# Performance work log

Hardware: AMD Instinct MI355X
Metric: run time of the kernel (lower is better)

## Reference

```python
import jax, jax.numpy as jnp
import numpy as np

N, D = 32768, 1024

def setup_inputs() -> dict:
    key = jax.random.key(0)
    k1, k2, k3 = jax.random.split(key, 3)
    elg = jax.random.normal(k1, (N, D), dtype=jnp.float32)
    eth = jax.random.normal(k2, (N, D), dtype=jnp.float32)
    weight = jax.random.normal(k3, (D, D), dtype=jnp.float32)
    return {"elg": elg, "eth": eth, "weight": weight}

def reference(elg, eth, weight):
    # out[n] = elg[n] @ W @ eth[n]  -- batched bilinear form, fully fused
    return jnp.einsum('nd,de,ne->n', elg, weight, eth)
```

## Files before the change

### kernel.cpp

```cpp
#include <hip/hip_runtime.h>
#include <hip/hip_bf16.h>

typedef __attribute__((ext_vector_type(8))) short short8;
typedef __attribute__((ext_vector_type(4))) float float4v;
typedef __attribute__((ext_vector_type(4))) unsigned int uint4v;

#define DDIM 1024
#define ETH_STRIDE 40

__device__ __forceinline__ unsigned short f2bf(float f) {
  unsigned u = __builtin_bit_cast(unsigned, f);
  unsigned r = (u + 0x7fffu + ((u >> 16) & 1u)) >> 16;
  return (unsigned short)r;
}
__device__ __forceinline__ unsigned pk2(float lo, float hi) {
  return (unsigned)f2bf(lo) | ((unsigned)f2bf(hi) << 16);
}

__global__ __launch_bounds__(256) void convert_w(const float* __restrict__ W,
                                                 unsigned short* __restrict__ Wb) {
  size_t i = ((size_t)blockIdx.x * 256 + threadIdx.x) * 8;
  float4v a = *(const float4v*)(W + i);
  float4v b = *(const float4v*)(W + i + 4);
  uint4v pk;
  pk.x = pk2(a.x, a.y); pk.y = pk2(a.z, a.w);
  pk.z = pk2(b.x, b.y); pk.w = pk2(b.z, b.w);
  *(uint4v*)(Wb + i) = pk;
}

__global__ __launch_bounds__(256, 3) void bilinear_kernel(const float* __restrict__ elg,
                                                          const float* __restrict__ eth,
                                                          const unsigned short* __restrict__ Wb,
                                                          float* __restrict__ out) {
  __shared__ unsigned short ethL[64 * ETH_STRIDE];
  __shared__ unsigned short Wbuf[256 * 32];
  __shared__ float wsum[4][64];

  const int tid  = threadIdx.x;
  const int lane = tid & 63;
  const int w    = tid >> 6;
  const int quad = lane >> 4;
  const int l15  = lane & 15;
  const int m0   = (blockIdx.x >> 2) * 64;
  const int d0   = (blockIdx.x & 3) * 256;

  const int erow = tid >> 2, eunit = tid & 3;
  const float* esrc = eth + (size_t)(m0 + erow) * DDIM + eunit * 8;

  const int wr = lane >> 2, wu = lane & 3;

  float4v er0 = *(const float4v*)(esrc);
  float4v er1 = *(const float4v*)(esrc + 4);

  float4v acc[4][4];
#pragma unroll
  for (int ct = 0; ct < 4; ++ct)
#pragma unroll
    for (int rt = 0; rt < 4; ++rt)
      acc[ct][rt] = (float4v){0.f, 0.f, 0.f, 0.f};

  for (int ek = 0; ek < 32; ++ek) {
    const int e0 = ek * 32;
    __syncthreads();

    {
      uint4v pk;
      pk.x = pk2(er0.x, er0.y); pk.y = pk2(er0.z, er0.w);
      pk.z = pk2(er1.x, er1.y); pk.w = pk2(er1.z, er1.w);
      *(uint4v*)&ethL[erow * ETH_STRIDE + eunit * 8] = pk;
    }

#pragma unroll
    for (int j = 0; j < 4; ++j) {
      int r  = (w * 4 + j) * 16 + wr;
      int ug = wu ^ ((r >> 1) & 3);
      const unsigned short* gp = Wb + (size_t)(d0 + r) * DDIM + e0 + ug * 8;
      unsigned short* lp = &Wbuf[(w * 4 + j) * 512 + lane * 8];
      __builtin_amdgcn_global_load_lds(
          (const __attribute__((address_space(1))) unsigned int*)gp,
          (__attribute__((address_space(3))) unsigned int*)lp, 16, 0, 0);
    }
    __syncthreads();

    short8 aF[4], bF[4];
#pragma unroll
    for (int rt = 0; rt < 4; ++rt)
      aF[rt] = *(const short8*)&ethL[(rt * 16 + l15) * ETH_STRIDE + quad * 8];
#pragma unroll
    for (int ct = 0; ct < 4; ++ct) {
      int dl = w * 64 + ct * 16 + l15;
      int pu = quad ^ ((dl >> 1) & 3);
      bF[ct] = *(const short8*)&Wbuf[dl * 32 + pu * 8];
    }

    if (ek < 31) {
      const float* s = esrc + (e0 + 32);
      er0 = *(const float4v*)(s);
      er1 = *(const float4v*)(s + 4);
    }

#pragma unroll
    for (int ct = 0; ct < 4; ++ct)
#pragma unroll
      for (int rt = 0; rt < 4; ++rt)
        acc[ct][rt] = __builtin_amdgcn_mfma_f32_16x16x32_bf16(aF[rt], bF[ct], acc[ct][rt], 0, 0, 0);
  }

  float p[16];
#pragma unroll
  for (int j = 0; j < 16; ++j) p[j] = 0.f;
#pragma unroll
  for (int ct = 0; ct < 4; ++ct) {
    int col = d0 + w * 64 + ct * 16 + l15;
#pragma unroll
    for (int rt = 0; rt < 4; ++rt) {
      const float* ep = elg + (size_t)(m0 + rt * 16 + quad * 4) * DDIM + col;
#pragma unroll
      for (int i = 0; i < 4; ++i)
        p[rt * 4 + i] += acc[ct][rt][i] * ep[(size_t)i * DDIM];
    }
  }

#pragma unroll
  for (int off = 1; off < 16; off <<= 1)
#pragma unroll
    for (int j = 0; j < 16; ++j)
      p[j] += __shfl_xor(p[j], off);

  if (l15 == 0) {
#pragma unroll
    for (int rt = 0; rt < 4; ++rt)
#pragma unroll
      for (int i = 0; i < 4; ++i)
        wsum[w][rt * 16 + quad * 4 + i] = p[rt * 4 + i];
  }
  __syncthreads();
  if (tid < 64) {
    float s = wsum[0][tid] + wsum[1][tid] + wsum[2][tid] + wsum[3][tid];
    atomicAdd(&out[m0 + tid], s);
  }
}

extern "C" void kernel_launch(void* const* d_in, const int* in_sizes, int n_in,
                              void* d_out, int out_size, void* d_ws, size_t ws_size,
                              hipStream_t stream) {
  (void)in_sizes; (void)n_in; (void)ws_size;
  const float* elg = (const float*)d_in[0];
  const float* eth = (const float*)d_in[1];
  const float* W   = (const float*)d_in[2];
  float* out = (float*)d_out;
  unsigned short* Wb = (unsigned short*)d_ws;

  hipMemsetAsync(d_out, 0, (size_t)out_size * sizeof(float), stream);
  convert_w<<<dim3(512), dim3(256), 0, stream>>>(W, Wb);
  bilinear_kernel<<<dim3(2048), dim3(256), 0, stream>>>(elg, eth, Wb, out);
}
```

Before: 368.3 us.

## Pre-convert eth to bf16 and double-buffer async LDS staging

Adds a combined conversion kernel that turns both W and eth into bf16 in workspace. The main kernel then streams both operands into LDS with global_load_lds, double-buffered so the next k-slice loads while MFMAs run on the current one, with one barrier per iteration. This removes the per-iteration fp32 register conversion and the second barrier. The cost is an extra 128MB read and 64MB write pass over eth, and a 64MB workspace requirement, with the old path kept as a fallback.

Measured after the change: 365.6 us. About the same (-0.7%).

```diff
diff --git a/kernel.cpp b/kernel.cpp
--- a/kernel.cpp
+++ b/kernel.cpp
@@ -16,24 +16,40 @@
 __device__ __forceinline__ unsigned pk2(float lo, float hi) {
   return (unsigned)f2bf(lo) | ((unsigned)f2bf(hi) << 16);
 }
-
+__device__ __forceinline__ void cvt8(const float* src, unsigned short* dst) {
+  float4v a = *(const float4v*)(src);
+  float4v b = *(const float4v*)(src + 4);
+  uint4v pk;
+  pk.x = pk2(a.x, a.y); pk.y = pk2(a.z, a.w);
+  pk.z = pk2(b.x, b.y); pk.w = pk2(b.z, b.w);
+  *(uint4v*)dst = pk;
+}
+
+__global__ __launch_bounds__(256) void convert_all(const float* __restrict__ W,
+                                                   const float* __restrict__ eth,
+                                                   unsigned short* __restrict__ Wb,
+                                                   unsigned short* __restrict__ ethB) {
+  int b = blockIdx.x;
+  if (b < 512) {
+    size_t i = ((size_t)b * 256 + threadIdx.x) * 8;
+    cvt8(W + i, Wb + i);
+  } else {
+    size_t i = ((size_t)(b - 512) * 256 + threadIdx.x) * 8;
+    cvt8(eth + i, ethB + i);
+  }
+}
 __global__ __launch_bounds__(256) void convert_w(const float* __restrict__ W,
                                                  unsigned short* __restrict__ Wb) {
   size_t i = ((size_t)blockIdx.x * 256 + threadIdx.x) * 8;
-  float4v a = *(const float4v*)(W + i);
-  float4v b = *(const float4v*)(W + i + 4);
-  uint4v pk;
-  pk.x = pk2(a.x, a.y); pk.y = pk2(a.z, a.w);
-  pk.z = pk2(b.x, b.y); pk.w = pk2(b.z, b.w);
-  *(uint4v*)(Wb + i) = pk;
-}
-
-__global__ __launch_bounds__(256, 3) void bilinear_kernel(const float* __restrict__ elg,
-                                                          const float* __restrict__ eth,
-                                                          const unsigned short* __restrict__ Wb,
-                                                          float* __restrict__ out) {
-  __shared__ unsigned short ethL[64 * ETH_STRIDE];
-  __shared__ unsigned short Wbuf[256 * 32];
+  cvt8(W + i, Wb + i);
+}
+
+__global__ __launch_bounds__(256, 3) void bilinear_bf16(const float* __restrict__ elg,
+                                                        const unsigned short* __restrict__ ethB,
+                                                        const unsigned short* __restrict__ Wb,
+                                                        float* __restrict__ out) {
+  __shared__ unsigned short Wbuf[2][256 * 32];
+  __shared__ unsigned short ethL[2][64 * 32];
   __shared__ float wsum[4][64];
 
   const int tid  = threadIdx.x;
@@ -43,33 +59,130 @@
   const int l15  = lane & 15;
   const int m0   = (blockIdx.x >> 2) * 64;
   const int d0   = (blockIdx.x & 3) * 256;
-
+  const int wr = lane >> 2, wu = lane & 3;
+
+  auto stage = [&](int ek, int buf) {
+    const int e0 = ek * 32;
+#pragma unroll
+    for (int j = 0; j < 4; ++j) {
+      int r  = (w * 4 + j) * 16 + wr;
+      int ug = wu ^ ((r >> 1) & 3);
+      const unsigned short* gp = Wb + (size_t)(d0 + r) * DDIM + e0 + ug * 8;
+      unsigned short* lp = &Wbuf[buf][(w * 4 + j) * 512 + lane * 8];
+      __builtin_amdgcn_global_load_lds(
+          (const __attribute__((address_space(1))) unsigned int*)gp,
+          (__attribute__((address_space(3))) unsigned int*)lp, 16, 0, 0);
+    }
+    {
+      int er = w * 16 + wr;
+      const unsigned short* gp = ethB + (size_t)(m0 + er) * DDIM + e0 + wu * 8;
+      unsigned short* lp = &ethL[buf][w * 512 + lane * 8];
+      __builtin_amdgcn_global_load_lds(
+          (const __attribute__((address_space(1))) unsigned int*)gp,
+          (__attribute__((address_space(3))) unsigned int*)lp, 16, 0, 0);
+    }
+  };
+
+  float4v acc[4][4];
+#pragma unroll
+  for (int ct = 0; ct < 4; ++ct)
+#pragma unroll
+    for (int rt = 0; rt < 4; ++rt)
+      acc[ct][rt] = (float4v){0.f, 0.f, 0.f, 0.f};
+
+  stage(0, 0);
+  __syncthreads();
+
+  for (int ek = 0; ek < 32; ++ek) {
+    const int cur = ek & 1;
+    if (ek < 31) stage(ek + 1, cur ^ 1);
+
+    short8 aF[4], bF[4];
+#pragma unroll
+    for (int rt = 0; rt < 4; ++rt)
+      aF[rt] = *(const short8*)&ethL[cur][(rt * 16 + l15) * 32 + quad * 8];
+#pragma unroll
+    for (int ct = 0; ct < 4; ++ct) {
+      int dl = w * 64 + ct * 16 + l15;
+      int pu = quad ^ ((dl >> 1) & 3);
+      bF[ct] = *(const short8*)&Wbuf[cur][dl * 32 + pu * 8];
+    }
+#pragma unroll
+    for (int ct = 0; ct < 4; ++ct)
+#pragma unroll
+      for (int rt = 0; rt < 4; ++rt)
+        acc[ct][rt] = __builtin_amdgcn_mfma_f32_16x16x32_bf16(aF[rt], bF[ct], acc[ct][rt], 0, 0, 0);
+
+    __syncthreads();
+  }
+
+  float p[16];
+#pragma unroll
+  for (int j = 0; j < 16; ++j) p[j] = 0.f;
+#pragma unroll
+  for (int ct = 0; ct < 4; ++ct) {
+    int col = d0 + w * 64 + ct * 16 + l15;
+#pragma unroll
+    for (int rt = 0; rt < 4; ++rt) {
+      const float* ep = elg + (size_t)(m0 + rt * 16 + quad * 4) * DDIM + col;
+#pragma unroll
+      for (int i = 0; i < 4; ++i)
+        p[rt * 4 + i] += acc[ct][rt][i] * ep[(size_t)i * DDIM];
+    }
+  }
+#pragma unroll
+  for (int off = 1; off < 16; off <<= 1)
+#pragma unroll
+    for (int j = 0; j < 16; ++j)
+      p[j] += __shfl_xor(p[j], off);
+  if (l15 == 0) {
+#pragma unroll
+    for (int rt = 0; rt < 4; ++rt)
+#pragma unroll
+      for (int i = 0; i < 4; ++i)
+        wsum[w][rt * 16 + quad * 4 + i] = p[rt * 4 + i];
+  }
+  __syncthreads();
+  if (tid < 64) {
+    float s = wsum[0][tid] + wsum[1][tid] + wsum[2][tid] + wsum[3][tid];
+    atomicAdd(&out[m0 + tid], s);
+  }
+}
+
+__global__ __launch_bounds__(256, 3) void bilinear_fp32eth(const float* __restrict__ elg,
+                                                           const float* __restrict__ eth,
+                                                           const unsigned short* __restrict__ Wb,
+                                                           float* __restrict__ out) {
+  __shared__ unsigned short ethL[64 * ETH_STRIDE];
+  __shared__ unsigned short Wbuf[256 * 32];
+  __shared__ float wsum[4][64];
+  const int tid  = threadIdx.x;
+  const int lane = tid & 63;
+  const int w    = tid >> 6;
+  const int quad = lane >> 4;
+  const int l15  = lane & 15;
+  const int m0   = (blockIdx.x >> 2) * 64;
+  const int d0   = (blockIdx.x & 3) * 256;
   const int erow = tid >> 2, eunit = tid & 3;
   const float* esrc = eth + (size_t)(m0 + erow) * DDIM + eunit * 8;
-
   const int wr = lane >> 2, wu = lane & 3;
-
   float4v er0 = *(const float4v*)(esrc);
   float4v er1 = *(const float4v*)(esrc + 4);
-
   float4v acc[4][4];
 #pragma unroll
   for (int ct = 0; ct < 4; ++ct)
 #pragma unroll
     for (int rt = 0; rt < 4; ++rt)
       acc[ct][rt] = (float4v){0.f, 0.f, 0.f, 0.f};
-
   for (int ek = 0; ek < 32; ++ek) {
     const int e0 = ek * 32;
     __syncthreads();
-
     {
       uint4v pk;
       pk.x = pk2(er0.x, er0.y); pk.y = pk2(er0.z, er0.w);
       pk.z = pk2(er1.x, er1.y); pk.w = pk2(er1.z, er1.w);
       *(uint4v*)&ethL[erow * ETH_STRIDE + eunit * 8] = pk;
     }
-
 #pragma unroll
     for (int j = 0; j < 4; ++j) {
       int r  = (w * 4 + j) * 16 + wr;
@@ -81,7 +194,6 @@
           (__attribute__((address_space(3))) unsigned int*)lp, 16, 0, 0);
     }
     __syncthreads();
-
     short8 aF[4], bF[4];
 #pragma unroll
     for (int rt = 0; rt < 4; ++rt)
@@ -92,20 +204,17 @@
       int pu = quad ^ ((dl >> 1) & 3);
       bF[ct] = *(const short8*)&Wbuf[dl * 32 + pu * 8];
     }
-
     if (ek < 31) {
       const float* s = esrc + (e0 + 32);
       er0 = *(const float4v*)(s);
       er1 = *(const float4v*)(s + 4);
     }
-
 #pragma unroll
     for (int ct = 0; ct < 4; ++ct)
 #pragma unroll
       for (int rt = 0; rt < 4; ++rt)
         acc[ct][rt] = __builtin_amdgcn_mfma_f32_16x16x32_bf16(aF[rt], bF[ct], acc[ct][rt], 0, 0, 0);
   }
-
   float p[16];
 #pragma unroll
   for (int j = 0; j < 16; ++j) p[j] = 0.f;
@@ -120,13 +229,11 @@
         p[rt * 4 + i] += acc[ct][rt][i] * ep[(size_t)i * DDIM];
     }
   }
-
 #pragma unroll
   for (int off = 1; off < 16; off <<= 1)
 #pragma unroll
     for (int j = 0; j < 16; ++j)
       p[j] += __shfl_xor(p[j], off);
-
   if (l15 == 0) {
 #pragma unroll
     for (int rt = 0; rt < 4; ++rt)
@@ -144,14 +251,21 @@
 extern "C" void kernel_launch(void* const* d_in, const int* in_sizes, int n_in,
                               void* d_out, int out_size, void* d_ws, size_t ws_size,
                               hipStream_t stream) {
-  (void)in_sizes; (void)n_in; (void)ws_size;
+  (void)in_sizes; (void)n_in;
   const float* elg = (const float*)d_in[0];
   const float* eth = (const float*)d_in[1];
   const float* W   = (const float*)d_in[2];
   float* out = (float*)d_out;
-  unsigned short* Wb = (unsigned short*)d_ws;
-
+  unsigned short* Wb   = (unsigned short*)d_ws;
+  unsigned short* ethB = (unsigned short*)((char*)d_ws + (2 << 20));
+
+  const size_t need = (2ull << 20) + (64ull << 20);
   hipMemsetAsync(d_out, 0, (size_t)out_size * sizeof(float), stream);
-  convert_w<<<dim3(512), dim3(256), 0, stream>>>(W, Wb);
-  bilinear_kernel<<<dim3(2048), dim3(256), 0, stream>>>(elg, eth, Wb, out);
-}
+  if (ws_size >= need) {
+    convert_all<<<dim3(512 + 16384), dim3(256), 0, stream>>>(W, eth, Wb, ethB);
+    bilinear_bf16<<<dim3(2048), dim3(256), 0, stream>>>(elg, ethB, Wb, out);
+  } else {
+    convert_w<<<dim3(512), dim3(256), 0, stream>>>(W, Wb);
+    bilinear_fp32eth<<<dim3(2048), dim3(256), 0, stream>>>(elg, eth, Wb, out);
+  }
+}
```
